# Kernel optimization log

Hardware: AMD Instinct MI355X
Metric: run time of the kernel (lower is better)

Reference implementation:

```python
import jax, jax.numpy as jnp
import numpy as np

WINDOW_SIZE = 32
SIM_THRESHOLD = 0.7
N_TOKENS = 262144
DIM = 256


def setup_inputs() -> dict:
    key = jax.random.key(0)
    x = jax.random.normal(key, (N_TOKENS, DIM), dtype=jnp.float32)
    return {"x": x}


def reference(x):
    """Stage 1 (global window pruning) + Stage 3 (sequential merge) of FocusModules.

    Returns:
      mask1: [N] bool keep-mask equivalent to compute_patch_similarity's index list
             (indices retained are exactly jnp.where(mask1)[0]).
      compressed: [N, D] float, features with stage-3-dropped tokens zeroed
             (mask-compacted form of spatial_token_compression's output; the
             retained rows in order equal the torch output).
    """
    N, D = x.shape
    W = WINDOW_SIZE
    nw = N // W  # N chosen as multiple of W

    # F.normalize(x, p=2, dim=-1) with eps clamp
    norms = jnp.maximum(jnp.linalg.norm(x, axis=-1, keepdims=True), 1e-12)
    xn = x / norms

    # ---- Stage 1: per-window cosine-similarity thresholding (vectorized over windows)
    win = xn.reshape(nw, W, D)
    sim = jnp.einsum('nwd,nvd->nwv', win, win)          # [nw, W, W]
    mean_sim = sim.mean(axis=2)                          # [nw, W]
    mu = mean_sim.mean(axis=1, keepdims=True)
    sd = mean_sim.std(axis=1, ddof=1, keepdims=True)     # torch .std() is unbiased
    keep = ~(mean_sim > (mu + sd))                       # [nw, W] bool
    # fallback: if a window keeps nothing, keep its argmin token
    any_kept = keep.any(axis=1, keepdims=True)
    fallback = jnp.arange(W)[None, :] == mean_sim.argmin(axis=1)[:, None]
    keep = jnp.where(any_kept, keep, fallback)
    mask1 = keep.reshape(N)

    # ---- Stage 3: adjacent-pair cosine similarity pruning
    sim_adj = jnp.sum(xn[:-1] * xn[1:], axis=-1)         # [N-1] (unit vectors -> dot = cosine)
    mask3 = jnp.concatenate([jnp.ones((1,), dtype=bool), sim_adj < SIM_THRESHOLD])
    compressed = x * mask3[:, None].astype(x.dtype)      # zeroed instead of compacted (jit-static shape)

    return mask1, compressed
```

## Files before the change

### kernel.cpp

```cpp
#include <hip/hip_runtime.h>
#include <math.h>

#define TOKW 32
#define DIMS 256

typedef float f4v __attribute__((ext_vector_type(4)));

__global__ __launch_bounds__(256) void focus_kernel(
    const float* __restrict__ x,
    float* __restrict__ out_mask,
    float* __restrict__ out_comp)
{
    const int tid  = threadIdx.x;
    const int w    = blockIdx.x;
    const int tok  = tid >> 3;
    const int lt   = tid & 7;
    const int wid  = tid >> 6;
    const int tw   = tok & 7;
    const int lane = tid & 63;

    __shared__ float sh_ws[4][DIMS];
    __shared__ float sh_bd[5][DIMS];
    __shared__ float sh_m[TOKW];

    const long long g0 = (long long)w * TOKW;
    const long long tokbase = (g0 + tok) * (DIMS / 4);
    const float4* xv = (const float4*)x;

    float4 v[8];
#pragma unroll
    for (int j = 0; j < 8; ++j)
        v[j] = xv[tokbase + lt + 8 * j];

    float4 pv = make_float4(0.f, 0.f, 0.f, 0.f);
    if (tid < 64 && w > 0) pv = xv[(g0 - 1) * (DIMS / 4) + tid];

    float ss = 0.f;
#pragma unroll
    for (int j = 0; j < 8; ++j)
        ss += v[j].x * v[j].x + v[j].y * v[j].y + v[j].z * v[j].z + v[j].w * v[j].w;
    ss += __shfl_xor(ss, 1);
    ss += __shfl_xor(ss, 2);
    ss += __shfl_xor(ss, 4);
    const float rn = 1.0f / fmaxf(sqrtf(ss), 1e-12f);

    float4 t[8];
#pragma unroll
    for (int j = 0; j < 8; ++j) {
        t[j].x = v[j].x * rn; t[j].y = v[j].y * rn;
        t[j].z = v[j].z * rn; t[j].w = v[j].w * rn;
    }

    if (tw == 7) {
#pragma unroll
        for (int j = 0; j < 8; ++j)
            *(float4*)&sh_bd[wid][4 * (lt + 8 * j)] = t[j];
    }

#pragma unroll
    for (int j = 0; j < 8; ++j) {
        t[j].x += __shfl_xor(t[j].x, 8);
        t[j].y += __shfl_xor(t[j].y, 8);
        t[j].z += __shfl_xor(t[j].z, 8);
        t[j].w += __shfl_xor(t[j].w, 8);
    }
#pragma unroll
    for (int j = 0; j < 8; ++j) {
        t[j].x += __shfl_xor(t[j].x, 16);
        t[j].y += __shfl_xor(t[j].y, 16);
        t[j].z += __shfl_xor(t[j].z, 16);
        t[j].w += __shfl_xor(t[j].w, 16);
    }
#pragma unroll
    for (int j = 0; j < 8; ++j) {
        t[j].x += __shfl_xor(t[j].x, 32);
        t[j].y += __shfl_xor(t[j].y, 32);
        t[j].z += __shfl_xor(t[j].z, 32);
        t[j].w += __shfl_xor(t[j].w, 32);
    }
    if (tw == 0) {
#pragma unroll
        for (int j = 0; j < 8; ++j)
            *(float4*)&sh_ws[wid][4 * (lt + 8 * j)] = t[j];
    }

    if (tid < 64) {
        float ps = pv.x * pv.x + pv.y * pv.y + pv.z * pv.z + pv.w * pv.w;
        ps += __shfl_xor(ps, 1);
        ps += __shfl_xor(ps, 2);
        ps += __shfl_xor(ps, 4);
        ps += __shfl_xor(ps, 8);
        ps += __shfl_xor(ps, 16);
        ps += __shfl_xor(ps, 32);
        const float prn = 1.0f / fmaxf(sqrtf(ps), 1e-12f);
        *(float4*)&sh_bd[4][tid * 4] =
            make_float4(pv.x * prn, pv.y * prn, pv.z * prn, pv.w * prn);
    }

    __syncthreads();

    {
        float dp = 0.f;
#pragma unroll
        for (int j = 0; j < 8; ++j) {
            const int f = 4 * (lt + 8 * j);
            const float4 s0 = *(const float4*)&sh_ws[0][f];
            const float4 s1 = *(const float4*)&sh_ws[1][f];
            const float4 s2 = *(const float4*)&sh_ws[2][f];
            const float4 s3 = *(const float4*)&sh_ws[3][f];
            dp += v[j].x * (s0.x + s1.x + s2.x + s3.x)
                + v[j].y * (s0.y + s1.y + s2.y + s3.y)
                + v[j].z * (s0.z + s1.z + s2.z + s3.z)
                + v[j].w * (s0.w + s1.w + s2.w + s3.w);
        }
        dp += __shfl_xor(dp, 1);
        dp += __shfl_xor(dp, 2);
        dp += __shfl_xor(dp, 4);
        if (lt == 0) sh_m[tok] = dp * rn * (1.0f / 32.0f);
    }

    const float prn_s = __shfl(rn, (lane - 8) & 63);
    float ap = 0.f;
#pragma unroll
    for (int j = 0; j < 8; ++j) {
        const float px = __shfl(v[j].x, (lane - 8) & 63);
        const float py = __shfl(v[j].y, (lane - 8) & 63);
        const float pz = __shfl(v[j].z, (lane - 8) & 63);
        const float pw = __shfl(v[j].w, (lane - 8) & 63);
        ap += px * v[j].x + py * v[j].y + pz * v[j].z + pw * v[j].w;
    }
    float pscale = prn_s;

    __syncthreads();

    if (tw == 0) {
        const float* prow = (tok == 0) ? sh_bd[4] : sh_bd[wid - 1];
        ap = 0.f;
#pragma unroll
        for (int j = 0; j < 8; ++j) {
            const float4 p4 = *(const float4*)&prow[4 * (lt + 8 * j)];
            ap += p4.x * v[j].x + p4.y * v[j].y + p4.z * v[j].z + p4.w * v[j].w;
        }
        pscale = 1.0f;
    }

    float mu = 0.f;
#pragma unroll
    for (int ti = 0; ti < TOKW; ++ti)
        mu += sh_m[ti];
    mu *= (1.0f / 32.0f);

    float var = 0.f;
#pragma unroll
    for (int ti = 0; ti < TOKW; ++ti) {
        float d = sh_m[ti] - mu;
        var += d * d;
    }
    var *= (1.0f / 31.0f);
    const float thr = mu + sqrtf(var);

    int cnt = 0, amin = 0;
    float mmin = sh_m[0];
#pragma unroll
    for (int ti = 0; ti < TOKW; ++ti) {
        float m = sh_m[ti];
        cnt += (m <= thr) ? 1 : 0;
        if (m < mmin) { mmin = m; amin = ti; }
    }

    if (tid < TOKW) {
        bool k = (cnt > 0) ? (sh_m[tid] <= thr) : (tid == amin);
        __builtin_nontemporal_store(k ? 1.0f : 0.0f, out_mask + g0 + tid);
    }

    float sim = ap;
    sim += __shfl_xor(sim, 1);
    sim += __shfl_xor(sim, 2);
    sim += __shfl_xor(sim, 4);
    sim *= rn * pscale;
    const float mult = (sim < 0.7f) ? 1.0f : 0.0f;

    f4v* ov = (f4v*)out_comp;
#pragma unroll
    for (int j = 0; j < 8; ++j) {
        f4v o;
        o.x = v[j].x * mult; o.y = v[j].y * mult;
        o.z = v[j].z * mult; o.w = v[j].w * mult;
        __builtin_nontemporal_store(o, ov + tokbase + lt + 8 * j);
    }
}

extern "C" void kernel_launch(void* const* d_in, const int* in_sizes, int n_in,
                              void* d_out, int out_size, void* d_ws, size_t ws_size,
                              hipStream_t stream) {
    const float* x = (const float*)d_in[0];
    const int ND = in_sizes[0];
    const int N  = ND / DIMS;
    const int nw = N / TOKW;

    float* out_mask = (float*)d_out;
    float* out_comp = out_mask + N;

    focus_kernel<<<nw, 256, 0, stream>>>(x, out_mask, out_comp);
}
```

Before: 451.5 us.

## Process four windows per block with register-prefetched next window

```diff
diff --git a/kernel.cpp b/kernel.cpp
--- a/kernel.cpp
+++ b/kernel.cpp
@@ -3,8 +3,7 @@
 
 #define TOKW 32
 #define DIMS 256
-
-typedef float f4v __attribute__((ext_vector_type(4)));
+#define WPB  4
 
 __global__ __launch_bounds__(256) void focus_kernel(
     const float* __restrict__ x,
@@ -12,181 +11,206 @@
     float* __restrict__ out_comp)
 {
     const int tid  = threadIdx.x;
-    const int w    = blockIdx.x;
     const int tok  = tid >> 3;
     const int lt   = tid & 7;
     const int wid  = tid >> 6;
     const int tw   = tok & 7;
     const int lane = tid & 63;
 
-    __shared__ float sh_ws[4][DIMS];
-    __shared__ float sh_bd[5][DIMS];
-    __shared__ float sh_m[TOKW];
-
-    const long long g0 = (long long)w * TOKW;
-    const long long tokbase = (g0 + tok) * (DIMS / 4);
+    __shared__ float sh_ws[2][4][DIMS];
+    __shared__ float sh_bd[WPB][4][DIMS];
+    __shared__ float sh_prev[DIMS];
+    __shared__ float sh_m[2][TOKW];
+
+    const int wbase = blockIdx.x * WPB;
     const float4* xv = (const float4*)x;
 
-    float4 v[8];
-#pragma unroll
-    for (int j = 0; j < 8; ++j)
-        v[j] = xv[tokbase + lt + 8 * j];
-
+    float4 cur[8];
+    {
+        const long long tb0 = ((long long)wbase * TOKW + tok) * (DIMS / 4);
+#pragma unroll
+        for (int j = 0; j < 8; ++j)
+            cur[j] = xv[tb0 + lt + 8 * j];
+    }
     float4 pv = make_float4(0.f, 0.f, 0.f, 0.f);
-    if (tid < 64 && w > 0) pv = xv[(g0 - 1) * (DIMS / 4) + tid];
-
-    float ss = 0.f;
-#pragma unroll
-    for (int j = 0; j < 8; ++j)
-        ss += v[j].x * v[j].x + v[j].y * v[j].y + v[j].z * v[j].z + v[j].w * v[j].w;
-    ss += __shfl_xor(ss, 1);
-    ss += __shfl_xor(ss, 2);
-    ss += __shfl_xor(ss, 4);
-    const float rn = 1.0f / fmaxf(sqrtf(ss), 1e-12f);
-
-    float4 t[8];
-#pragma unroll
-    for (int j = 0; j < 8; ++j) {
-        t[j].x = v[j].x * rn; t[j].y = v[j].y * rn;
-        t[j].z = v[j].z * rn; t[j].w = v[j].w * rn;
-    }
-
-    if (tw == 7) {
+    if (tid < 64 && wbase > 0)
+        pv = xv[((long long)wbase * TOKW - 1) * (DIMS / 4) + tid];
+
+#pragma unroll
+    for (int i = 0; i < WPB; ++i) {
+        const int b = i & 1;
+        const long long g0 = (long long)(wbase + i) * TOKW;
+        const long long tokbase = (g0 + tok) * (DIMS / 4);
+
+        float4 nxt[8];
+        if (i + 1 < WPB) {
+            const long long tbn = tokbase + TOKW * (DIMS / 4);
+#pragma unroll
+            for (int j = 0; j < 8; ++j)
+                nxt[j] = xv[tbn + lt + 8 * j];
+        }
+
+        float ss = 0.f;
 #pragma unroll
         for (int j = 0; j < 8; ++j)
-            *(float4*)&sh_bd[wid][4 * (lt + 8 * j)] = t[j];
-    }
-
-#pragma unroll
-    for (int j = 0; j < 8; ++j) {
-        t[j].x += __shfl_xor(t[j].x, 8);
-        t[j].y += __shfl_xor(t[j].y, 8);
-        t[j].z += __shfl_xor(t[j].z, 8);
-        t[j].w += __shfl_xor(t[j].w, 8);
-    }
-#pragma unroll
-    for (int j = 0; j < 8; ++j) {
-        t[j].x += __shfl_xor(t[j].x, 16);
-        t[j].y += __shfl_xor(t[j].y, 16);
-        t[j].z += __shfl_xor(t[j].z, 16);
-        t[j].w += __shfl_xor(t[j].w, 16);
-    }
-#pragma unroll
-    for (int j = 0; j < 8; ++j) {
-        t[j].x += __shfl_xor(t[j].x, 32);
-        t[j].y += __shfl_xor(t[j].y, 32);
-        t[j].z += __shfl_xor(t[j].z, 32);
-        t[j].w += __shfl_xor(t[j].w, 32);
-    }
-    if (tw == 0) {
-#pragma unroll
-        for (int j = 0; j < 8; ++j)
-            *(float4*)&sh_ws[wid][4 * (lt + 8 * j)] = t[j];
-    }
-
-    if (tid < 64) {
-        float ps = pv.x * pv.x + pv.y * pv.y + pv.z * pv.z + pv.w * pv.w;
-        ps += __shfl_xor(ps, 1);
-        ps += __shfl_xor(ps, 2);
-        ps += __shfl_xor(ps, 4);
-        ps += __shfl_xor(ps, 8);
-        ps += __shfl_xor(ps, 16);
-        ps += __shfl_xor(ps, 32);
-        const float prn = 1.0f / fmaxf(sqrtf(ps), 1e-12f);
-        *(float4*)&sh_bd[4][tid * 4] =
-            make_float4(pv.x * prn, pv.y * prn, pv.z * prn, pv.w * prn);
-    }
-
-    __syncthreads();
-
-    {
-        float dp = 0.f;
-#pragma unroll
-        for (int j = 0; j < 8; ++j) {
-            const int f = 4 * (lt + 8 * j);
-            const float4 s0 = *(const float4*)&sh_ws[0][f];
-            const float4 s1 = *(const float4*)&sh_ws[1][f];
-            const float4 s2 = *(const float4*)&sh_ws[2][f];
-            const float4 s3 = *(const float4*)&sh_ws[3][f];
-            dp += v[j].x * (s0.x + s1.x + s2.x + s3.x)
-                + v[j].y * (s0.y + s1.y + s2.y + s3.y)
-                + v[j].z * (s0.z + s1.z + s2.z + s3.z)
-                + v[j].w * (s0.w + s1.w + s2.w + s3.w);
-        }
-        dp += __shfl_xor(dp, 1);
-        dp += __shfl_xor(dp, 2);
-        dp += __shfl_xor(dp, 4);
-        if (lt == 0) sh_m[tok] = dp * rn * (1.0f / 32.0f);
-    }
-
-    const float prn_s = __shfl(rn, (lane - 8) & 63);
-    float ap = 0.f;
-#pragma unroll
-    for (int j = 0; j < 8; ++j) {
-        const float px = __shfl(v[j].x, (lane - 8) & 63);
-        const float py = __shfl(v[j].y, (lane - 8) & 63);
-        const float pz = __shfl(v[j].z, (lane - 8) & 63);
-        const float pw = __shfl(v[j].w, (lane - 8) & 63);
-        ap += px * v[j].x + py * v[j].y + pz * v[j].z + pw * v[j].w;
-    }
-    float pscale = prn_s;
-
-    __syncthreads();
-
-    if (tw == 0) {
-        const float* prow = (tok == 0) ? sh_bd[4] : sh_bd[wid - 1];
-        ap = 0.f;
-#pragma unroll
-        for (int j = 0; j < 8; ++j) {
-            const float4 p4 = *(const float4*)&prow[4 * (lt + 8 * j)];
-            ap += p4.x * v[j].x + p4.y * v[j].y + p4.z * v[j].z + p4.w * v[j].w;
-        }
-        pscale = 1.0f;
-    }
-
-    float mu = 0.f;
-#pragma unroll
-    for (int ti = 0; ti < TOKW; ++ti)
-        mu += sh_m[ti];
-    mu *= (1.0f / 32.0f);
-
-    float var = 0.f;
-#pragma unroll
-    for (int ti = 0; ti < TOKW; ++ti) {
-        float d = sh_m[ti] - mu;
-        var += d * d;
-    }
-    var *= (1.0f / 31.0f);
-    const float thr = mu + sqrtf(var);
-
-    int cnt = 0, amin = 0;
-    float mmin = sh_m[0];
-#pragma unroll
-    for (int ti = 0; ti < TOKW; ++ti) {
-        float m = sh_m[ti];
-        cnt += (m <= thr) ? 1 : 0;
-        if (m < mmin) { mmin = m; amin = ti; }
-    }
-
-    if (tid < TOKW) {
-        bool k = (cnt > 0) ? (sh_m[tid] <= thr) : (tid == amin);
-        __builtin_nontemporal_store(k ? 1.0f : 0.0f, out_mask + g0 + tid);
-    }
-
-    float sim = ap;
-    sim += __shfl_xor(sim, 1);
-    sim += __shfl_xor(sim, 2);
-    sim += __shfl_xor(sim, 4);
-    sim *= rn * pscale;
-    const float mult = (sim < 0.7f) ? 1.0f : 0.0f;
-
-    f4v* ov = (f4v*)out_comp;
-#pragma unroll
-    for (int j = 0; j < 8; ++j) {
-        f4v o;
-        o.x = v[j].x * mult; o.y = v[j].y * mult;
-        o.z = v[j].z * mult; o.w = v[j].w * mult;
-        __builtin_nontemporal_store(o, ov + tokbase + lt + 8 * j);
+            ss += cur[j].x * cur[j].x + cur[j].y * cur[j].y
+                + cur[j].z * cur[j].z + cur[j].w * cur[j].w;
+        ss += __shfl_xor(ss, 1);
+        ss += __shfl_xor(ss, 2);
+        ss += __shfl_xor(ss, 4);
+        const float rn = 1.0f / fmaxf(sqrtf(ss), 1e-12f);
+
+        float4 t[8];
+#pragma unroll
+        for (int j = 0; j < 8; ++j) {
+            t[j].x = cur[j].x * rn; t[j].y = cur[j].y * rn;
+            t[j].z = cur[j].z * rn; t[j].w = cur[j].w * rn;
+        }
+        if (tw == 7) {
+#pragma unroll
+            for (int j = 0; j < 8; ++j)
+                *(float4*)&sh_bd[i][wid][4 * (lt + 8 * j)] = t[j];
+        }
+
+#pragma unroll
+        for (int j = 0; j < 8; ++j) {
+            t[j].x += __shfl_xor(t[j].x, 8);
+            t[j].y += __shfl_xor(t[j].y, 8);
+            t[j].z += __shfl_xor(t[j].z, 8);
+            t[j].w += __shfl_xor(t[j].w, 8);
+        }
+#pragma unroll
+        for (int j = 0; j < 8; ++j) {
+            t[j].x += __shfl_xor(t[j].x, 16);
+            t[j].y += __shfl_xor(t[j].y, 16);
+            t[j].z += __shfl_xor(t[j].z, 16);
+            t[j].w += __shfl_xor(t[j].w, 16);
+        }
+#pragma unroll
+        for (int j = 0; j < 8; ++j) {
+            t[j].x += __shfl_xor(t[j].x, 32);
+            t[j].y += __shfl_xor(t[j].y, 32);
+            t[j].z += __shfl_xor(t[j].z, 32);
+            t[j].w += __shfl_xor(t[j].w, 32);
+        }
+        if (tw == 0) {
+#pragma unroll
+            for (int j = 0; j < 8; ++j)
+                *(float4*)&sh_ws[b][wid][4 * (lt + 8 * j)] = t[j];
+        }
+
+        if (i == 0 && tid < 64) {
+            float ps = pv.x * pv.x + pv.y * pv.y + pv.z * pv.z + pv.w * pv.w;
+            ps += __shfl_xor(ps, 1);
+            ps += __shfl_xor(ps, 2);
+            ps += __shfl_xor(ps, 4);
+            ps += __shfl_xor(ps, 8);
+            ps += __shfl_xor(ps, 16);
+            ps += __shfl_xor(ps, 32);
+            const float prn = 1.0f / fmaxf(sqrtf(ps), 1e-12f);
+            *(float4*)&sh_prev[tid * 4] =
+                make_float4(pv.x * prn, pv.y * prn, pv.z * prn, pv.w * prn);
+        }
+
+        __syncthreads();
+
+        {
+            float dp = 0.f;
+#pragma unroll
+            for (int j = 0; j < 8; ++j) {
+                const int f = 4 * (lt + 8 * j);
+                const float4 s0 = *(const float4*)&sh_ws[b][0][f];
+                const float4 s1 = *(const float4*)&sh_ws[b][1][f];
+                const float4 s2 = *(const float4*)&sh_ws[b][2][f];
+                const float4 s3 = *(const float4*)&sh_ws[b][3][f];
+                dp += cur[j].x * (s0.x + s1.x + s2.x + s3.x)
+                    + cur[j].y * (s0.y + s1.y + s2.y + s3.y)
+                    + cur[j].z * (s0.z + s1.z + s2.z + s3.z)
+                    + cur[j].w * (s0.w + s1.w + s2.w + s3.w);
+            }
+            dp += __shfl_xor(dp, 1);
+            dp += __shfl_xor(dp, 2);
+            dp += __shfl_xor(dp, 4);
+            if (lt == 0) sh_m[b][tok] = dp * rn * (1.0f / 32.0f);
+        }
+
+        const float prn_s = __shfl(rn, (lane - 8) & 63);
+        float ap = 0.f;
+#pragma unroll
+        for (int j = 0; j < 8; ++j) {
+            const float px = __shfl(cur[j].x, (lane - 8) & 63);
+            const float py = __shfl(cur[j].y, (lane - 8) & 63);
+            const float pz = __shfl(cur[j].z, (lane - 8) & 63);
+            const float pw = __shfl(cur[j].w, (lane - 8) & 63);
+            ap += px * cur[j].x + py * cur[j].y + pz * cur[j].z + pw * cur[j].w;
+        }
+        float pscale = prn_s;
+
+        __syncthreads();
+
+        if (tw == 0) {
+            const float* prow = (tok == 0)
+                ? ((i == 0) ? sh_prev : sh_bd[i - 1][3])
+                : sh_bd[i][wid - 1];
+            ap = 0.f;
+#pragma unroll
+            for (int j = 0; j < 8; ++j) {
+                const float4 p4 = *(const float4*)&prow[4 * (lt + 8 * j)];
+                ap += p4.x * cur[j].x + p4.y * cur[j].y
+                    + p4.z * cur[j].z + p4.w * cur[j].w;
+            }
+            pscale = 1.0f;
+        }
+
+        float mu = 0.f;
+#pragma unroll
+        for (int ti = 0; ti < TOKW; ++ti)
+            mu += sh_m[b][ti];
+        mu *= (1.0f / 32.0f);
+
+        float var = 0.f;
+#pragma unroll
+        for (int ti = 0; ti < TOKW; ++ti) {
+            float d = sh_m[b][ti] - mu;
+            var += d * d;
+        }
+        var *= (1.0f / 31.0f);
+        const float thr = mu + sqrtf(var);
+
+        int cnt = 0, amin = 0;
+        float mmin = sh_m[b][0];
+#pragma unroll
+        for (int ti = 0; ti < TOKW; ++ti) {
+            float m = sh_m[b][ti];
+            cnt += (m <= thr) ? 1 : 0;
+            if (m < mmin) { mmin = m; amin = ti; }
+        }
+
+        if (tid < TOKW) {
+            bool k = (cnt > 0) ? (sh_m[b][tid] <= thr) : (tid == amin);
+            out_mask[g0 + tid] = k ? 1.0f : 0.0f;
+        }
+
+        float sim = ap;
+        sim += __shfl_xor(sim, 1);
+        sim += __shfl_xor(sim, 2);
+        sim += __shfl_xor(sim, 4);
+        sim *= rn * pscale;
+        const float mult = (sim < 0.7f) ? 1.0f : 0.0f;
+
+        float4* ov = (float4*)out_comp;
+#pragma unroll
+        for (int j = 0; j < 8; ++j) {
+            float4 o = make_float4(cur[j].x * mult, cur[j].y * mult,
+                                   cur[j].z * mult, cur[j].w * mult);
+            ov[tokbase + lt + 8 * j] = o;
+        }
+
+        if (i + 1 < WPB) {
+#pragma unroll
+            for (int j = 0; j < 8; ++j)
+                cur[j] = nxt[j];
+        }
     }
 }
 
@@ -197,9 +221,10 @@
     const int ND = in_sizes[0];
     const int N  = ND / DIMS;
     const int nw = N / TOKW;
+    const int nb = nw / WPB;
 
     float* out_mask = (float*)d_out;
     float* out_comp = out_mask + N;
 
-    focus_kernel<<<nw, 256, 0, stream>>>(x, out_mask, out_comp);
+    focus_kernel<<<nb, 256, 0, stream>>>(x, out_mask, out_comp);
 }
```

Result: faster. 441.1 us (-2.3%).
